# Kernel optimization log

Hardware: AMD Instinct MI355X
Metric: run time of the kernel (lower is better)

Reference implementation:

```python
import jax, jax.numpy as jnp
import numpy as np

H = 256  # hidden_size


def setup_inputs() -> dict:
    key = jax.random.key(0)
    ks = jax.random.split(key, 9)
    std = 1.0 / np.sqrt(H)
    u = lambda k, shape: jax.random.uniform(k, shape, jnp.float32, -std, std)
    x = jax.random.normal(ks[0], (64, 16, 128, 64), jnp.float32)
    return {
        "x": x,
        "wi0": u(ks[1], (64, 3 * H)),
        "wh0": u(ks[2], (H, 3 * H)),
        "bi0": u(ks[3], (3 * H,)),
        "bh0": u(ks[4], (3 * H,)),
        "wi1": u(ks[5], (H, 3 * H)),
        "wh1": u(ks[6], (H, 3 * H)),
        "bi1": u(ks[7], (3 * H,)),
        "bh1": u(ks[8], (3 * H,)),
    }


def _cell(x_t, h, wi, wh, bi, bh):
    # x_t: (B, N, D), h: (B, N, H). Gates concatenated as [r|z|n].
    gi = x_t @ wi + bi           # (B, N, 3H)
    gh = h @ wh + bh             # (B, N, 3H)
    ir, iz, inn = jnp.split(gi, 3, axis=-1)
    hr, hz, hn = jnp.split(gh, 3, axis=-1)
    r = jax.nn.sigmoid(ir + hr)
    z = jax.nn.sigmoid(iz + hz)
    n = jnp.tanh(inn + r * hn)
    return (1.0 - z) * n + z * h


def reference(x, wi0, wh0, bi0, bh0, wi1, wh1, bi1, bh1):
    seq_len, B, N, _ = x.shape
    h0 = jnp.zeros((B, N, H), x.dtype)
    h1 = jnp.zeros((B, N, H), x.dtype)

    def step(carry, x_t):
        h0, h1 = carry
        h0 = _cell(x_t, h0, wi0, wh0, bi0, bh0)
        h1 = _cell(h0, h1, wi1, wh1, bi1, bh1)
        return (h0, h1), h1

    (h0, h1), output = jax.lax.scan(step, (h0, h1), x)
    hidden_out = jnp.stack([h0, h1], axis=0)  # (num_layers, B, N, H)
    return output, hidden_out
```

## Files before the change

### kernel.cpp

```cpp
#include <hip/hip_runtime.h>


typedef __attribute__((ext_vector_type(8))) __bf16 bf8;
typedef __attribute__((ext_vector_type(8))) unsigned short u16x8;
typedef __attribute__((ext_vector_type(4))) float f32x4;

#define MFMA16(A, B, C) __builtin_amdgcn_mfma_f32_16x16x32_bf16((A), (B), (C), 0, 0, 0)

#define ROWS 2048
#define HID 256
#define NW 768
#define SLOT (ROWS * HID)
#define OUT_HID_OFF ((size_t)64 * ROWS * HID)
#define R0SLOT 524288

static __device__ __forceinline__ float b2f(unsigned short u) {
  union { unsigned u32; float f; } v;
  v.u32 = ((unsigned)u) << 16;
  return v.f;
}
static __device__ __forceinline__ unsigned short f2b(float f) {
  unsigned u = __float_as_uint(f);
  u += 0x7fffu + ((u >> 16) & 1u);
  return (unsigned short)(u >> 16);
}
static __device__ __forceinline__ float sigm(float x) {
  return 1.0f / (1.0f + __expf(-x));
}
static __device__ __forceinline__ float tanh_fast(float x) {
  x = fminf(15.0f, fmaxf(-15.0f, x));
  float e = __expf(2.0f * x);
  return (e - 1.0f) / (e + 1.0f);
}
static __device__ __forceinline__ float ldin(const void* p, int i, int f32w) {
  return f32w ? ((const float*)p)[i] : b2f(((const unsigned short*)p)[i]);
}
static __device__ __forceinline__ void stout(void* p, size_t i, float v, int f32w) {
  if (f32w) ((float*)p)[i] = v;
  else ((unsigned short*)p)[i] = f2b(v);
}

static __device__ __forceinline__ u16x8 ld_h16(const unsigned short* p) {
  union { unsigned long long q[2]; u16x8 b; } u;
  u.q[0] = __hip_atomic_load((const unsigned long long*)p, __ATOMIC_RELAXED,
                             __HIP_MEMORY_SCOPE_AGENT);
  u.q[1] = __hip_atomic_load((const unsigned long long*)(p + 4), __ATOMIC_RELAXED,
                             __HIP_MEMORY_SCOPE_AGENT);
  return u.b;
}
static __device__ __forceinline__ void st_h16(unsigned short* p, u16x8 v) {
  union { u16x8 s; unsigned long long q[2]; } u;
  u.s = v;
  __hip_atomic_store((unsigned long long*)p, u.q[0], __ATOMIC_RELAXED,
                     __HIP_MEMORY_SCOPE_AGENT);
  __hip_atomic_store((unsigned long long*)(p + 4), u.q[1], __ATOMIC_RELAXED,
                     __HIP_MEMORY_SCOPE_AGENT);
}

__global__ void probe_dtype(const unsigned short* x, unsigned* flag) {
  if (blockIdx.x != 0 || threadIdx.x != 0) return;
  int cnt = 0;
  for (int i = 0; i < 256; ++i) {
    float v = b2f(x[i]);
    if (v == v && fabsf(v) <= 8.0f) cnt++;
  }
  *flag = (cnt >= 250) ? 0u : 1u;
}

__global__ void pack_w(const void* __restrict__ W,
                       unsigned short* __restrict__ P, int KK,
                       const unsigned* __restrict__ flag) {
  int i = blockIdx.x * blockDim.x + threadIdx.x;
  int total = 48 * KK * 64;
  if (i >= total) return;
  int f32w = (int)*flag;
  int l = i & 63;
  int kk = (i >> 6) % KK;
  int nb = i / (64 * KK);
  int n = nb * 16 + (l & 15);
  int k0 = kk * 32 + (l >> 4) * 8;
  u16x8 tmp;
#pragma unroll
  for (int e = 0; e < 8; ++e) tmp[e] = f2b(ldin(W, (k0 + e) * NW + n, f32w));
  *(u16x8*)(P + (size_t)i * 8) = tmp;
}

__global__ void __launch_bounds__(256, 1) gru_main(
    const void* __restrict__ x,
    const void* __restrict__ bi0, const void* __restrict__ bh0,
    const void* __restrict__ bi1, const void* __restrict__ bh1,
    const unsigned short* __restrict__ pwi0, const unsigned short* __restrict__ pwh0,
    const unsigned short* __restrict__ pwi1, const unsigned short* __restrict__ pwh1,
    void* __restrict__ out,
    unsigned short* __restrict__ ring0, unsigned short* __restrict__ ring1,
    unsigned* __restrict__ flags, const unsigned* __restrict__ flag) {
  __shared__ __align__(16) unsigned short AS[16384];
  __shared__ __align__(16) unsigned short HS[2][2304];

  const int f32w = (int)*flag;
  const int tid = threadIdx.x;
  const int lane = tid & 63;
  const int wid = tid >> 6;
  const int bid = blockIdx.x;
  const int g = bid & 63;
  const int slice = bid >> 6;
  const int nb = slice * 4 + wid;

  const int d = nb * 16 + (lane & 15);
  const int rb = g * 32;
  const int arow = rb + (lane & 15);
  const int koff = (lane >> 4) * 8;
  const int rl = (lane >> 4) * 4;
  const int cl = wid * 16 + (lane & 15);

  unsigned* flagp = flags + (size_t)g * 64;

  const unsigned short* xw  = pwi0 + (size_t)nb * 1024;
  const unsigned short* w0  = pwh0 + (size_t)nb * 4096;
  const unsigned short* w1i = pwi1 + (size_t)nb * 4096;
  const unsigned short* w1h = pwh1 + (size_t)nb * 4096;

  const float iR0 = ldin(bi0, d, f32w) + ldin(bh0, d, f32w);
  const float iZ0 = ldin(bi0, 256 + d, f32w) + ldin(bh0, 256 + d, f32w);
  const float iI0 = ldin(bi0, 512 + d, f32w);
  const float iH0 = ldin(bh0, 512 + d, f32w);
  const float iR1 = ldin(bi1, d, f32w) + ldin(bh1, d, f32w);
  const float iZ1 = ldin(bi1, 256 + d, f32w) + ldin(bh1, 256 + d, f32w);
  const float iI1 = ldin(bi1, 512 + d, f32w);
  const float iH1 = ldin(bh1, 512 + d, f32w);

  float h0p[2][4] = {{0, 0, 0, 0}, {0, 0, 0, 0}};
  float h1p[2][4] = {{0, 0, 0, 0}, {0, 0, 0, 0}};

  const int ef = tid >> 7;
  const int ekk = (tid >> 6) & 1;
  const int eln = tid & 63;
  const int ehs = (ef * 16 + (eln & 15)) * 72 + ekk * 32 + (eln >> 4) * 8;
  const size_t ero = (size_t)g * 8192 +
                     (size_t)(ef * 8 + slice * 2 + ekk) * 512 + eln * 8;

  for (int t = 0; t <= 64; ++t) {
    const int sc = t & 1;
    const int sp = sc ^ 1;

    f32x4 aR0[2], aZ0[2], aI0[2], aH0[2], aR1[2], aZ1[2], aI1[2], aH1[2];
#pragma unroll
    for (int f = 0; f < 2; ++f) {
      aR0[f] = (f32x4){iR0, iR0, iR0, iR0};
      aZ0[f] = (f32x4){iZ0, iZ0, iZ0, iZ0};
      aI0[f] = (f32x4){iI0, iI0, iI0, iI0};
      aH0[f] = (f32x4){iH0, iH0, iH0, iH0};
      aR1[f] = (f32x4){iR1, iR1, iR1, iR1};
      aZ1[f] = (f32x4){iZ1, iZ1, iZ1, iZ1};
      aI1[f] = (f32x4){iI1, iI1, iI1, iI1};
      aH1[f] = (f32x4){iH1, iH1, iH1, iH1};
    }

    if (t < 64) {
      size_t xoff = ((size_t)t * ROWS + arow) * 64 + koff;
#pragma unroll
      for (int kk = 0; kk < 2; ++kk) {
        union { u16x8 u; bf8 b; } A0, A1;
        if (f32w) {
          const float* ab = (const float*)x + xoff;
#pragma unroll
          for (int e = 0; e < 8; ++e) {
            A0.u[e] = f2b(ab[kk * 32 + e]);
            A1.u[e] = f2b(ab[16 * 64 + kk * 32 + e]);
          }
        } else {
          const unsigned short* ab = (const unsigned short*)x + xoff;
          A0.u = *(const u16x8*)(ab + kk * 32);
          A1.u = *(const u16x8*)(ab + 16 * 64 + kk * 32);
        }
        const int lb = lane * 8;
        bf8 Br = *(const bf8*)(xw + 0 * 16384 + kk * 512 + lb);
        bf8 Bz = *(const bf8*)(xw + 1 * 16384 + kk * 512 + lb);
        bf8 Bn = *(const bf8*)(xw + 2 * 16384 + kk * 512 + lb);
        aR0[0] = MFMA16(A0.b, Br, aR0[0]);
        aR0[1] = MFMA16(A1.b, Br, aR0[1]);
        aZ0[0] = MFMA16(A0.b, Bz, aZ0[0]);
        aZ0[1] = MFMA16(A1.b, Bz, aZ0[1]);
        aI0[0] = MFMA16(A0.b, Bn, aI0[0]);
        aI0[1] = MFMA16(A1.b, Bn, aI0[1]);
      }
    }

    if (t > 0 && tid == 0) {
      const unsigned tgt = 4u * (unsigned)t;
      while (__hip_atomic_load(flagp, __ATOMIC_RELAXED,
                               __HIP_MEMORY_SCOPE_AGENT) < tgt)
        __builtin_amdgcn_s_sleep(1);
    }
    __syncthreads();

    {
      const unsigned short* r0 = ring0 + (size_t)sp * R0SLOT + (size_t)g * 8192;
#pragma unroll
      for (int i = 0; i < 4; ++i) {
        int idx = tid + i * 256;
        int ff = idx >> 6, ln2 = idx & 63;
        *(u16x8*)(AS + ff * 512 + ln2 * 8) = ld_h16(r0 + ff * 512 + ln2 * 8);
      }
      if (t >= 2) {
        const unsigned short* r1 = ring1 + (size_t)sc * R0SLOT + (size_t)g * 8192;
#pragma unroll
        for (int i = 0; i < 4; ++i) {
          int idx = tid + i * 256;
          int ff = idx >> 6, ln2 = idx & 63;
          *(u16x8*)(AS + 8192 + ff * 512 + ln2 * 8) =
              ld_h16(r1 + ff * 512 + ln2 * 8);
        }
      }
    }
    __syncthreads();

#pragma unroll
    for (int kk = 0; kk < 8; ++kk) {
      const int lb = lane * 8;
      bf8 A0 = *(const bf8*)(AS + (0 * 8 + kk) * 512 + lb);
      bf8 A1 = *(const bf8*)(AS + (1 * 8 + kk) * 512 + lb);
      bf8 Br0 = *(const bf8*)(w0 + 0 * 65536 + kk * 512 + lb);
      bf8 Bz0 = *(const bf8*)(w0 + 1 * 65536 + kk * 512 + lb);
      bf8 Bn0 = *(const bf8*)(w0 + 2 * 65536 + kk * 512 + lb);
      bf8 Br1 = *(const bf8*)(w1i + 0 * 65536 + kk * 512 + lb);
      bf8 Bz1 = *(const bf8*)(w1i + 1 * 65536 + kk * 512 + lb);
      bf8 Bn1 = *(const bf8*)(w1i + 2 * 65536 + kk * 512 + lb);
      aR0[0] = MFMA16(A0, Br0, aR0[0]);
      aR0[1] = MFMA16(A1, Br0, aR0[1]);
      aZ0[0] = MFMA16(A0, Bz0, aZ0[0]);
      aZ0[1] = MFMA16(A1, Bz0, aZ0[1]);
      aH0[0] = MFMA16(A0, Bn0, aH0[0]);
      aH0[1] = MFMA16(A1, Bn0, aH0[1]);
      aR1[0] = MFMA16(A0, Br1, aR1[0]);
      aR1[1] = MFMA16(A1, Br1, aR1[1]);
      aZ1[0] = MFMA16(A0, Bz1, aZ1[0]);
      aZ1[1] = MFMA16(A1, Bz1, aZ1[1]);
      aI1[0] = MFMA16(A0, Bn1, aI1[0]);
      aI1[1] = MFMA16(A1, Bn1, aI1[1]);
    }
    if (t >= 2) {
#pragma unroll
      for (int kk = 0; kk < 8; ++kk) {
        const int lb = lane * 8;
        bf8 A0 = *(const bf8*)(AS + 8192 + (0 * 8 + kk) * 512 + lb);
        bf8 A1 = *(const bf8*)(AS + 8192 + (1 * 8 + kk) * 512 + lb);
        bf8 Br = *(const bf8*)(w1h + 0 * 65536 + kk * 512 + lb);
        bf8 Bz = *(const bf8*)(w1h + 1 * 65536 + kk * 512 + lb);
        bf8 Bn = *(const bf8*)(w1h + 2 * 65536 + kk * 512 + lb);
        aR1[0] = MFMA16(A0, Br, aR1[0]);
        aR1[1] = MFMA16(A1, Br, aR1[1]);
        aZ1[0] = MFMA16(A0, Bz, aZ1[0]);
        aZ1[1] = MFMA16(A1, Bz, aZ1[1]);
        aH1[0] = MFMA16(A0, Bn, aH1[0]);
        aH1[1] = MFMA16(A1, Bn, aH1[1]);
      }
    }

    if (t < 64) {
#pragma unroll
      for (int f = 0; f < 2; ++f) {
#pragma unroll
        for (int j = 0; j < 4; ++j) {
          float r = sigm(aR0[f][j]);
          float z = sigm(aZ0[f][j]);
          float n = tanh_fast(aI0[f][j] + r * aH0[f][j]);
          float hv = (1.0f - z) * n + z * h0p[f][j];
          h0p[f][j] = hv;
          HS[0][(f * 16 + rl + j) * 72 + cl] = f2b(hv);
        }
      }
    }
    if (t >= 1) {
#pragma unroll
      for (int f = 0; f < 2; ++f) {
#pragma unroll
        for (int j = 0; j < 4; ++j) {
          float r = sigm(aR1[f][j]);
          float z = sigm(aZ1[f][j]);
          float n = tanh_fast(aI1[f][j] + r * aH1[f][j]);
          float hv = (1.0f - z) * n + z * h1p[f][j];
          h1p[f][j] = hv;
          HS[1][(f * 16 + rl + j) * 72 + cl] = f2b(hv);
        }
      }
    }
    __syncthreads();

    if (t < 64) {
      st_h16(ring0 + (size_t)sc * R0SLOT + ero, *(const u16x8*)(&HS[0][ehs]));
      if (t >= 1)
        st_h16(ring1 + (size_t)sp * R0SLOT + ero, *(const u16x8*)(&HS[1][ehs]));
    }

    asm volatile("s_waitcnt vmcnt(0)" ::: "memory");
    __syncthreads();
    if (t < 64 && tid == 0)
      __hip_atomic_fetch_add(flagp, 1u, __ATOMIC_RELAXED,
                             __HIP_MEMORY_SCOPE_AGENT);

    if (t >= 1) {
      const int tm1 = t - 1;
#pragma unroll
      for (int f = 0; f < 2; ++f) {
#pragma unroll
        for (int j = 0; j < 4; ++j) {
          int row = rb + f * 16 + rl + j;
          stout(out, ((size_t)tm1 * ROWS + row) * HID + d, h1p[f][j], f32w);
          if (tm1 == 63)
            stout(out, OUT_HID_OFF + (size_t)SLOT + (size_t)row * HID + d,
                  h1p[f][j], f32w);
        }
      }
    }
    if (t == 63) {
#pragma unroll
      for (int f = 0; f < 2; ++f) {
#pragma unroll
        for (int j = 0; j < 4; ++j) {
          int row = rb + f * 16 + rl + j;
          stout(out, OUT_HID_OFF + (size_t)row * HID + d, h0p[f][j], f32w);
        }
      }
    }
  }
}

extern "C" void kernel_launch(void* const* d_in, const int* in_sizes, int n_in,
                              void* d_out, int out_size, void* d_ws, size_t ws_size,
                              hipStream_t stream) {
  (void)in_sizes; (void)n_in; (void)out_size; (void)ws_size;
  const void* x   = d_in[0];
  const void* wi0 = d_in[1];
  const void* wh0 = d_in[2];
  const void* bi0 = d_in[3];
  const void* bh0 = d_in[4];
  const void* wi1 = d_in[5];
  const void* wh1 = d_in[6];
  const void* bi1 = d_in[7];
  const void* bh1 = d_in[8];
  void* out = d_out;

  char* ws = (char*)d_ws;
  unsigned* flags = (unsigned*)ws;
  unsigned* flag  = (unsigned*)(ws + 16384);
  unsigned short* ring0 = (unsigned short*)(ws + 32768);
  unsigned short* ring1 = (unsigned short*)(ws + 32768 + 2097152);
  unsigned short* pwi0 = (unsigned short*)(ws + 32768 + 4194304);
  unsigned short* pwh0 = pwi0 + 49152;
  unsigned short* pwi1 = pwh0 + 196608;
  unsigned short* pwh1 = pwi1 + 196608;

  hipMemsetAsync(d_ws, 0, 32768 + 2097152, stream);

  probe_dtype<<<1, 64, 0, stream>>>((const unsigned short*)x, flag);

  pack_w<<<(48 * 2 * 64 + 255) / 256, 256, 0, stream>>>(wi0, pwi0, 2, flag);
  pack_w<<<(48 * 8 * 64 + 255) / 256, 256, 0, stream>>>(wh0, pwh0, 8, flag);
  pack_w<<<(48 * 8 * 64 + 255) / 256, 256, 0, stream>>>(wi1, pwi1, 8, flag);
  pack_w<<<(48 * 8 * 64 + 255) / 256, 256, 0, stream>>>(wh1, pwh1, 8, flag);

  void* kargs[] = {&x, &bi0, &bh0, &bi1, &bh1, &pwi0, &pwh0, &pwi1, &pwh1,
                   &out, &ring0, &ring1, &flags, &flag};
  hipError_t lerr = hipLaunchCooperativeKernel(
      (const void*)gru_main, dim3(256), dim3(256), kargs, 0, stream);
  if (lerr != hipSuccess) {
    (void)hipGetLastError();
    gru_main<<<dim3(256), dim3(256), 0, stream>>>(
        x, bi0, bh0, bi1, bh1, pwi0, pwh0, pwi1, pwh1,
        out, ring0, ring1, flags, flag);
  }
}
```

Before: 703.9 us.

## Use XCC-local cache-scoped ring loads/stores and skip zero-state GEMM at t=0

Each group of four blocks checks whether all its members sit on the same XCC. If they do, the ring buffers for the hidden state are loaded and stored with sc0-only cache bits, so the traffic can stay in the XCC-local L2 instead of going to device scope. The ring loads become single dwordx4 inline-asm loads that are all issued before one drain, replacing pairs of 64-bit atomics. The t=0 GEMM on the all-zero state is skipped, so the memset now clears only the flags. This relies on the XCC-id detection and on cache-coherence assumptions that hold only when a group lives on one XCC.

```diff
diff --git a/kernel.cpp b/kernel.cpp
--- a/kernel.cpp
+++ b/kernel.cpp
@@ -3,6 +3,7 @@
 
 typedef __attribute__((ext_vector_type(8))) __bf16 bf8;
 typedef __attribute__((ext_vector_type(8))) unsigned short u16x8;
+typedef __attribute__((ext_vector_type(4))) unsigned u32x4;
 typedef __attribute__((ext_vector_type(4))) float f32x4;
 
 #define MFMA16(A, B, C) __builtin_amdgcn_mfma_f32_16x16x32_bf16((A), (B), (C), 0, 0, 0)
@@ -40,22 +41,25 @@
   else ((unsigned short*)p)[i] = f2b(v);
 }
 
-static __device__ __forceinline__ u16x8 ld_h16(const unsigned short* p) {
-  union { unsigned long long q[2]; u16x8 b; } u;
-  u.q[0] = __hip_atomic_load((const unsigned long long*)p, __ATOMIC_RELAXED,
-                             __HIP_MEMORY_SCOPE_AGENT);
-  u.q[1] = __hip_atomic_load((const unsigned long long*)(p + 4), __ATOMIC_RELAXED,
-                             __HIP_MEMORY_SCOPE_AGENT);
-  return u.b;
-}
-static __device__ __forceinline__ void st_h16(unsigned short* p, u16x8 v) {
-  union { u16x8 s; unsigned long long q[2]; } u;
-  u.s = v;
-  __hip_atomic_store((unsigned long long*)p, u.q[0], __ATOMIC_RELAXED,
-                     __HIP_MEMORY_SCOPE_AGENT);
-  __hip_atomic_store((unsigned long long*)(p + 4), u.q[1], __ATOMIC_RELAXED,
-                     __HIP_MEMORY_SCOPE_AGENT);
-}
+static __device__ __forceinline__ u32x4 ld16c(const void* p, int fast) {
+  u32x4 r;
+  if (fast)
+    asm volatile("global_load_dwordx4 %0, %1, off sc0"
+                 : "=v"(r) : "v"(p) : "memory");
+  else
+    asm volatile("global_load_dwordx4 %0, %1, off sc0 sc1"
+                 : "=v"(r) : "v"(p) : "memory");
+  return r;
+}
+static __device__ __forceinline__ void st16c(void* p, u32x4 v, int fast) {
+  if (fast)
+    asm volatile("global_store_dwordx4 %0, %1, off sc0"
+                 : : "v"(p), "v"(v) : "memory");
+  else
+    asm volatile("global_store_dwordx4 %0, %1, off sc0 sc1"
+                 : : "v"(p), "v"(v) : "memory");
+}
+#define VMDRAIN asm volatile("s_waitcnt vmcnt(0)" ::: "memory")
 
 __global__ void probe_dtype(const unsigned short* x, unsigned* flag) {
   if (blockIdx.x != 0 || threadIdx.x != 0) return;
@@ -115,6 +119,22 @@
 
   unsigned* flagp = flags + (size_t)g * 64;
 
+  unsigned xcc;
+  asm volatile("s_getreg_b32 %0, hwreg(HW_REG_XCC_ID)" : "=s"(xcc));
+  if (tid == 0) {
+    __hip_atomic_fetch_or(flagp + 32, 1u << (xcc & 31u), __ATOMIC_RELAXED,
+                          __HIP_MEMORY_SCOPE_AGENT);
+    __hip_atomic_fetch_add(flagp + 33, 1u, __ATOMIC_RELEASE,
+                           __HIP_MEMORY_SCOPE_AGENT);
+    while (__hip_atomic_load(flagp + 33, __ATOMIC_RELAXED,
+                             __HIP_MEMORY_SCOPE_AGENT) < 4u)
+      __builtin_amdgcn_s_sleep(1);
+  }
+  __syncthreads();
+  const unsigned xmask = __hip_atomic_load(flagp + 32, __ATOMIC_RELAXED,
+                                           __HIP_MEMORY_SCOPE_AGENT);
+  const int fast = (xmask != 0u) && ((xmask & (xmask - 1u)) == 0u);
+
   const unsigned short* xw  = pwi0 + (size_t)nb * 1024;
   const unsigned short* w0  = pwh0 + (size_t)nb * 4096;
   const unsigned short* w1i = pwi1 + (size_t)nb * 4096;
@@ -195,49 +215,70 @@
     __syncthreads();
 
     {
-      const unsigned short* r0 = ring0 + (size_t)sp * R0SLOT + (size_t)g * 8192;
-#pragma unroll
-      for (int i = 0; i < 4; ++i) {
-        int idx = tid + i * 256;
-        int ff = idx >> 6, ln2 = idx & 63;
-        *(u16x8*)(AS + ff * 512 + ln2 * 8) = ld_h16(r0 + ff * 512 + ln2 * 8);
-      }
-      if (t >= 2) {
-        const unsigned short* r1 = ring1 + (size_t)sc * R0SLOT + (size_t)g * 8192;
+      u32x4 t0[4], t1[4];
+      if (t >= 1) {
+        const unsigned short* r0 = ring0 + (size_t)sp * R0SLOT + (size_t)g * 8192;
 #pragma unroll
         for (int i = 0; i < 4; ++i) {
           int idx = tid + i * 256;
           int ff = idx >> 6, ln2 = idx & 63;
-          *(u16x8*)(AS + 8192 + ff * 512 + ln2 * 8) =
-              ld_h16(r1 + ff * 512 + ln2 * 8);
+          t0[i] = ld16c(r0 + ff * 512 + ln2 * 8, fast);
+        }
+      }
+      if (t >= 2) {
+        const unsigned short* r1 = ring1 + (size_t)sc * R0SLOT + (size_t)g * 8192;
+#pragma unroll
+        for (int i = 0; i < 4; ++i) {
+          int idx = tid + i * 256;
+          int ff = idx >> 6, ln2 = idx & 63;
+          t1[i] = ld16c(r1 + ff * 512 + ln2 * 8, fast);
+        }
+      }
+      VMDRAIN;
+      if (t >= 1) {
+#pragma unroll
+        for (int i = 0; i < 4; ++i) {
+          int idx = tid + i * 256;
+          int ff = idx >> 6, ln2 = idx & 63;
+          *(u32x4*)(AS + ff * 512 + ln2 * 8) = t0[i];
+        }
+      }
+      if (t >= 2) {
+#pragma unroll
+        for (int i = 0; i < 4; ++i) {
+          int idx = tid + i * 256;
+          int ff = idx >> 6, ln2 = idx & 63;
+          *(u32x4*)(AS + 8192 + ff * 512 + ln2 * 8) = t1[i];
         }
       }
     }
     __syncthreads();
 
-#pragma unroll
-    for (int kk = 0; kk < 8; ++kk) {
-      const int lb = lane * 8;
-      bf8 A0 = *(const bf8*)(AS + (0 * 8 + kk) * 512 + lb);
-      bf8 A1 = *(const bf8*)(AS + (1 * 8 + kk) * 512 + lb);
-      bf8 Br0 = *(const bf8*)(w0 + 0 * 65536 + kk * 512 + lb);
-      bf8 Bz0 = *(const bf8*)(w0 + 1 * 65536 + kk * 512 + lb);
-      bf8 Bn0 = *(const bf8*)(w0 + 2 * 65536 + kk * 512 + lb);
-      bf8 Br1 = *(const bf8*)(w1i + 0 * 65536 + kk * 512 + lb);
-      bf8 Bz1 = *(const bf8*)(w1i + 1 * 65536 + kk * 512 + lb);
-      bf8 Bn1 = *(const bf8*)(w1i + 2 * 65536 + kk * 512 + lb);
-      aR0[0] = MFMA16(A0, Br0, aR0[0]);
-      aR0[1] = MFMA16(A1, Br0, aR0[1]);
-      aZ0[0] = MFMA16(A0, Bz0, aZ0[0]);
-      aZ0[1] = MFMA16(A1, Bz0, aZ0[1]);
-      aH0[0] = MFMA16(A0, Bn0, aH0[0]);
-      aH0[1] = MFMA16(A1, Bn0, aH0[1]);
-      aR1[0] = MFMA16(A0, Br1, aR1[0]);
-      aR1[1] = MFMA16(A1, Br1, aR1[1]);
-      aZ1[0] = MFMA16(A0, Bz1, aZ1[0]);
-      aZ1[1] = MFMA16(A1, Bz1, aZ1[1]);
-      aI1[0] = MFMA16(A0, Bn1, aI1[0]);
-      aI1[1] = MFMA16(A1, Bn1, aI1[1]);
+    if (t >= 1) {
+#pragma unroll
+      for (int kk = 0; kk < 8; ++kk) {
+        const int lb = lane * 8;
+        bf8 A0 = *(const bf8*)(AS + (0 * 8 + kk) * 512 + lb);
+        bf8 A1 = *(const bf8*)(AS + (1 * 8 + kk) * 512 + lb);
+        bf8 Br0 = *(const bf8*)(w0 + 0 * 65536 + kk * 512 + lb);
+        bf8 Bz0 = *(const bf8*)(w0 + 1 * 65536 + kk * 512 + lb);
+        bf8 Bn0 = *(const bf8*)(w0 + 2 * 65536 + kk * 512 + lb);
+        bf8 Br1 = *(const bf8*)(w1i + 0 * 65536 + kk * 512 + lb);
+        bf8 Bz1 = *(const bf8*)(w1i + 1 * 65536 + kk * 512 + lb);
+        bf8 Bn1 = *(const bf8*)(w1i + 2 * 65536 + kk * 512 + lb);
+        aR0[0] = MFMA16(A0, Br0, aR0[0]);
+        aR0[1] = MFMA16(A1, Br0, aR0[1]);
+        aZ0[0] = MFMA16(A0, Bz0, aZ0[0]);
+        aZ0[1] = MFMA16(A1, Bz0, aZ0[1]);
+        aH0[0] = MFMA16(A0, Bn0, aH0[0]);
+        aH0[1] = MFMA16(A1, Bn0, aH0[1]);
+        aR1[0] = MFMA16(A0, Br1, aR1[0]);
+        aR1[1] = MFMA16(A1, Br1, aR1[1]);
+        aZ1[0] = MFMA16(A0, Bz1, aZ1[0]);
+        aZ1[1] = MFMA16(A1, Bz1, aZ1[1]);
+        aI1[0] = MFMA16(A0, Bn1, aI1[0]);
+        aI1[1] = MFMA16(A1, Bn1, aI1[1]);
+      }
     }
     if (t >= 2) {
 #pragma unroll
@@ -288,12 +329,12 @@
     __syncthreads();
 
     if (t < 64) {
-      st_h16(ring0 + (size_t)sc * R0SLOT + ero, *(const u16x8*)(&HS[0][ehs]));
+      st16c(ring0 + (size_t)sc * R0SLOT + ero, *(const u32x4*)(&HS[0][ehs]), fast);
       if (t >= 1)
-        st_h16(ring1 + (size_t)sp * R0SLOT + ero, *(const u16x8*)(&HS[1][ehs]));
-    }
-
-    asm volatile("s_waitcnt vmcnt(0)" ::: "memory");
+        st16c(ring1 + (size_t)sp * R0SLOT + ero, *(const u32x4*)(&HS[1][ehs]), fast);
+    }
+
+    VMDRAIN;
     __syncthreads();
     if (t < 64 && tid == 0)
       __hip_atomic_fetch_add(flagp, 1u, __ATOMIC_RELAXED,
@@ -351,7 +392,7 @@
   unsigned short* pwi1 = pwh0 + 196608;
   unsigned short* pwh1 = pwi1 + 196608;
 
-  hipMemsetAsync(d_ws, 0, 32768 + 2097152, stream);
+  hipMemsetAsync(d_ws, 0, 16384 + 64, stream);
 
   probe_dtype<<<1, 64, 0, stream>>>((const unsigned short*)x, flag);
 
```

New measurement: 833.3 us. +18.4%, slower.

## Split per-layer sync flags and publish layer-0 state before layer-1 compute

Applied to the files above, without the earlier changes.

Replaces the single per-group completion flag with separate flags for layer 0 and layer 1. Each block now computes layer 0, publishes its h0 slice and signals flag0, and only then computes and publishes layer 1 and signals flag1. The aim is to let other blocks start the next timestep's layer-0 recurrence sooner, shortening the critical path across the wavefront pipeline. The cost is an extra barrier, an extra memory fence and store round, and a second spin-wait per step.

```diff
diff --git a/kernel.cpp b/kernel.cpp
--- a/kernel.cpp
+++ b/kernel.cpp
@@ -113,7 +113,8 @@
   const int rl = (lane >> 4) * 4;
   const int cl = wid * 16 + (lane & 15);
 
-  unsigned* flagp = flags + (size_t)g * 64;
+  unsigned* flag0p = flags + (size_t)g * 64;
+  unsigned* flag1p = flag0p + 32;
 
   const unsigned short* xw  = pwi0 + (size_t)nb * 1024;
   const unsigned short* w0  = pwh0 + (size_t)nb * 4096;
@@ -186,11 +187,19 @@
       }
     }
 
-    if (t > 0 && tid == 0) {
-      const unsigned tgt = 4u * (unsigned)t;
-      while (__hip_atomic_load(flagp, __ATOMIC_RELAXED,
-                               __HIP_MEMORY_SCOPE_AGENT) < tgt)
-        __builtin_amdgcn_s_sleep(1);
+    if (tid == 0) {
+      if (t >= 1) {
+        const unsigned tgt = 4u * (unsigned)t;
+        while (__hip_atomic_load(flag0p, __ATOMIC_RELAXED,
+                                 __HIP_MEMORY_SCOPE_AGENT) < tgt)
+          __builtin_amdgcn_s_sleep(1);
+      }
+      if (t >= 2) {
+        const unsigned tgt = 4u * (unsigned)(t - 1);
+        while (__hip_atomic_load(flag1p, __ATOMIC_RELAXED,
+                                 __HIP_MEMORY_SCOPE_AGENT) < tgt)
+          __builtin_amdgcn_s_sleep(1);
+      }
     }
     __syncthreads();
 
@@ -215,49 +224,22 @@
     }
     __syncthreads();
 
-#pragma unroll
-    for (int kk = 0; kk < 8; ++kk) {
-      const int lb = lane * 8;
-      bf8 A0 = *(const bf8*)(AS + (0 * 8 + kk) * 512 + lb);
-      bf8 A1 = *(const bf8*)(AS + (1 * 8 + kk) * 512 + lb);
-      bf8 Br0 = *(const bf8*)(w0 + 0 * 65536 + kk * 512 + lb);
-      bf8 Bz0 = *(const bf8*)(w0 + 1 * 65536 + kk * 512 + lb);
-      bf8 Bn0 = *(const bf8*)(w0 + 2 * 65536 + kk * 512 + lb);
-      bf8 Br1 = *(const bf8*)(w1i + 0 * 65536 + kk * 512 + lb);
-      bf8 Bz1 = *(const bf8*)(w1i + 1 * 65536 + kk * 512 + lb);
-      bf8 Bn1 = *(const bf8*)(w1i + 2 * 65536 + kk * 512 + lb);
-      aR0[0] = MFMA16(A0, Br0, aR0[0]);
-      aR0[1] = MFMA16(A1, Br0, aR0[1]);
-      aZ0[0] = MFMA16(A0, Bz0, aZ0[0]);
-      aZ0[1] = MFMA16(A1, Bz0, aZ0[1]);
-      aH0[0] = MFMA16(A0, Bn0, aH0[0]);
-      aH0[1] = MFMA16(A1, Bn0, aH0[1]);
-      aR1[0] = MFMA16(A0, Br1, aR1[0]);
-      aR1[1] = MFMA16(A1, Br1, aR1[1]);
-      aZ1[0] = MFMA16(A0, Bz1, aZ1[0]);
-      aZ1[1] = MFMA16(A1, Bz1, aZ1[1]);
-      aI1[0] = MFMA16(A0, Bn1, aI1[0]);
-      aI1[1] = MFMA16(A1, Bn1, aI1[1]);
-    }
-    if (t >= 2) {
+    if (t < 64) {
 #pragma unroll
       for (int kk = 0; kk < 8; ++kk) {
         const int lb = lane * 8;
-        bf8 A0 = *(const bf8*)(AS + 8192 + (0 * 8 + kk) * 512 + lb);
-        bf8 A1 = *(const bf8*)(AS + 8192 + (1 * 8 + kk) * 512 + lb);
-        bf8 Br = *(const bf8*)(w1h + 0 * 65536 + kk * 512 + lb);
-        bf8 Bz = *(const bf8*)(w1h + 1 * 65536 + kk * 512 + lb);
-        bf8 Bn = *(const bf8*)(w1h + 2 * 65536 + kk * 512 + lb);
-        aR1[0] = MFMA16(A0, Br, aR1[0]);
-        aR1[1] = MFMA16(A1, Br, aR1[1]);
-        aZ1[0] = MFMA16(A0, Bz, aZ1[0]);
-        aZ1[1] = MFMA16(A1, Bz, aZ1[1]);
-        aH1[0] = MFMA16(A0, Bn, aH1[0]);
-        aH1[1] = MFMA16(A1, Bn, aH1[1]);
-      }
-    }
-
-    if (t < 64) {
+        bf8 A0 = *(const bf8*)(AS + (0 * 8 + kk) * 512 + lb);
+        bf8 A1 = *(const bf8*)(AS + (1 * 8 + kk) * 512 + lb);
+        bf8 Br0 = *(const bf8*)(w0 + 0 * 65536 + kk * 512 + lb);
+        bf8 Bz0 = *(const bf8*)(w0 + 1 * 65536 + kk * 512 + lb);
+        bf8 Bn0 = *(const bf8*)(w0 + 2 * 65536 + kk * 512 + lb);
+        aR0[0] = MFMA16(A0, Br0, aR0[0]);
+        aR0[1] = MFMA16(A1, Br0, aR0[1]);
+        aZ0[0] = MFMA16(A0, Bz0, aZ0[0]);
+        aZ0[1] = MFMA16(A1, Bz0, aZ0[1]);
+        aH0[0] = MFMA16(A0, Bn0, aH0[0]);
+        aH0[1] = MFMA16(A1, Bn0, aH0[1]);
+      }
 #pragma unroll
       for (int f = 0; f < 2; ++f) {
 #pragma unroll
@@ -271,7 +253,49 @@
         }
       }
     }
+    __syncthreads();
+
+    if (t < 64)
+      st_h16(ring0 + (size_t)sc * R0SLOT + ero, *(const u16x8*)(&HS[0][ehs]));
+    asm volatile("s_waitcnt vmcnt(0)" ::: "memory");
+    __syncthreads();
+    if (t < 64 && tid == 0)
+      __hip_atomic_fetch_add(flag0p, 1u, __ATOMIC_RELAXED,
+                             __HIP_MEMORY_SCOPE_AGENT);
+
     if (t >= 1) {
+#pragma unroll
+      for (int kk = 0; kk < 8; ++kk) {
+        const int lb = lane * 8;
+        bf8 A0 = *(const bf8*)(AS + (0 * 8 + kk) * 512 + lb);
+        bf8 A1 = *(const bf8*)(AS + (1 * 8 + kk) * 512 + lb);
+        bf8 Br1 = *(const bf8*)(w1i + 0 * 65536 + kk * 512 + lb);
+        bf8 Bz1 = *(const bf8*)(w1i + 1 * 65536 + kk * 512 + lb);
+        bf8 Bn1 = *(const bf8*)(w1i + 2 * 65536 + kk * 512 + lb);
+        aR1[0] = MFMA16(A0, Br1, aR1[0]);
+        aR1[1] = MFMA16(A1, Br1, aR1[1]);
+        aZ1[0] = MFMA16(A0, Bz1, aZ1[0]);
+        aZ1[1] = MFMA16(A1, Bz1, aZ1[1]);
+        aI1[0] = MFMA16(A0, Bn1, aI1[0]);
+        aI1[1] = MFMA16(A1, Bn1, aI1[1]);
+      }
+      if (t >= 2) {
+#pragma unroll
+        for (int kk = 0; kk < 8; ++kk) {
+          const int lb = lane * 8;
+          bf8 A0 = *(const bf8*)(AS + 8192 + (0 * 8 + kk) * 512 + lb);
+          bf8 A1 = *(const bf8*)(AS + 8192 + (1 * 8 + kk) * 512 + lb);
+          bf8 Br = *(const bf8*)(w1h + 0 * 65536 + kk * 512 + lb);
+          bf8 Bz = *(const bf8*)(w1h + 1 * 65536 + kk * 512 + lb);
+          bf8 Bn = *(const bf8*)(w1h + 2 * 65536 + kk * 512 + lb);
+          aR1[0] = MFMA16(A0, Br, aR1[0]);
+          aR1[1] = MFMA16(A1, Br, aR1[1]);
+          aZ1[0] = MFMA16(A0, Bz, aZ1[0]);
+          aZ1[1] = MFMA16(A1, Bz, aZ1[1]);
+          aH1[0] = MFMA16(A0, Bn, aH1[0]);
+          aH1[1] = MFMA16(A1, Bn, aH1[1]);
+        }
+      }
 #pragma unroll
       for (int f = 0; f < 2; ++f) {
 #pragma unroll
@@ -287,16 +311,12 @@
     }
     __syncthreads();
 
-    if (t < 64) {
-      st_h16(ring0 + (size_t)sc * R0SLOT + ero, *(const u16x8*)(&HS[0][ehs]));
-      if (t >= 1)
-        st_h16(ring1 + (size_t)sp * R0SLOT + ero, *(const u16x8*)(&HS[1][ehs]));
-    }
-
+    if (t >= 1 && t < 64)
+      st_h16(ring1 + (size_t)sp * R0SLOT + ero, *(const u16x8*)(&HS[1][ehs]));
     asm volatile("s_waitcnt vmcnt(0)" ::: "memory");
     __syncthreads();
-    if (t < 64 && tid == 0)
-      __hip_atomic_fetch_add(flagp, 1u, __ATOMIC_RELAXED,
+    if (t >= 1 && t < 64 && tid == 0)
+      __hip_atomic_fetch_add(flag1p, 1u, __ATOMIC_RELAXED,
                              __HIP_MEMORY_SCOPE_AGENT);
 
     if (t >= 1) {
```

Measured after the change: 758.4 us. +7.7%, slower.
